# Kernel optimization log

Hardware: AMD Instinct MI355X
Metric: run time of the kernel (lower is better)

## Reference

```python
import jax, jax.numpy as jnp
import numpy as np

D_MODEL = 1024
N_HEADS = 16
D_HEAD = D_MODEL // N_HEADS
B, T = 4, 2048


def setup_inputs() -> dict:
    key = jax.random.key(0)
    ks = jax.random.split(key, 7)
    s = 0.02
    q = jax.random.normal(ks[0], (B, T, D_MODEL), dtype=jnp.float32)
    k = jax.random.normal(ks[1], (B, T, D_MODEL), dtype=jnp.float32)
    v = jax.random.normal(ks[2], (B, T, D_MODEL), dtype=jnp.float32)
    # causal mask, True = masked (strict upper triangle)
    mask = jnp.triu(jnp.ones((T, T), dtype=bool), k=1)[None, None, :, :]
    Wq = jax.random.normal(ks[3], (D_MODEL, D_MODEL), dtype=jnp.float32) * s
    Wk = jax.random.normal(ks[4], (D_MODEL, D_MODEL), dtype=jnp.float32) * s
    Wv = jax.random.normal(ks[5], (D_MODEL, D_MODEL), dtype=jnp.float32) * s
    Wo = jax.random.normal(ks[6], (D_MODEL, D_MODEL), dtype=jnp.float32) * s
    return {"q": q, "k": k, "v": v, "mask": mask,
            "Wq": Wq, "Wk": Wk, "Wv": Wv, "Wo": Wo}


def reference(q, k, v, mask, Wq, Wk, Wv, Wo):
    H, Dh = N_HEADS, D_HEAD
    scale = Dh ** -0.5

    def split(t):  # [B,T,D] -> [B,H,T,Dh]
        Bt, Tt, _ = t.shape
        return t.reshape(Bt, Tt, H, Dh).transpose(0, 2, 1, 3)

    # torch Linear (no bias): y = x @ W.T
    Q = split(q @ Wq.T)
    K = split(k @ Wk.T)
    V = split(v @ Wv.T)

    scores = jnp.einsum('bhqd,bhkd->bhqk', Q, K) * scale
    scores = jnp.where(mask, -jnp.inf, scores)
    attn = jax.nn.softmax(scores, axis=-1)
    attn = jnp.nan_to_num(attn)  # fully-masked rows -> 0
    out = jnp.einsum('bhqk,bhkd->bhqd', attn, V)
    out = out.transpose(0, 2, 1, 3).reshape(q.shape[0], q.shape[1], H * Dh)
    return out @ Wo.T
```

## Files before the change

### kernel.cpp

```cpp
#include <hip/hip_runtime.h>
#include <stdint.h>

#define D_MODEL 1024
#define N_HEADS 16
#define D_HEAD 64
#define BATCH 4
#define SEQ 2048
#define MTOT (BATCH * SEQ)

typedef unsigned short u16;
typedef __attribute__((ext_vector_type(8))) short bf16x8;
typedef __attribute__((ext_vector_type(4))) float f32x4;

#define MFMA(a, b, c) __builtin_amdgcn_mfma_f32_16x16x32_bf16((a), (b), (c), 0, 0, 0)
#define LOG2E 1.4426950408889634f
#define SC (0.125f * LOG2E)

static __device__ __forceinline__ u16 f2bf(float f) {
  unsigned u = __builtin_bit_cast(unsigned, f);
  u += 0x7fffu + ((u >> 16) & 1u);
  return (u16)(u >> 16);
}
static __device__ __forceinline__ u16 f2bf_t(float f) {
  return (u16)(__builtin_bit_cast(unsigned, f) >> 16);
}

static __device__ __forceinline__ void gload_lds16(const void* g, void* l) {
  __builtin_amdgcn_global_load_lds(
      (const __attribute__((address_space(1))) void*)g,
      (__attribute__((address_space(3))) void*)l, 16, 0, 0);
}

__global__ __launch_bounds__(256) void cvt3(const float* __restrict__ a,
                                            const float* __restrict__ b,
                                            const float* __restrict__ c,
                                            u16* __restrict__ oa, u16* __restrict__ ob,
                                            u16* __restrict__ oc) {
  const int z = blockIdx.y;
  const float* in = (z == 0) ? a : (z == 1) ? b : c;
  u16* out = (z == 0) ? oa : (z == 1) ? ob : oc;
  int i = blockIdx.x * 256 + threadIdx.x;
  float4 v = ((const float4*)in)[i];
  ushort4 o;
  o.x = f2bf(v.x); o.y = f2bf(v.y); o.z = f2bf(v.z); o.w = f2bf(v.w);
  ((ushort4*)out)[i] = o;
}

__global__ __launch_bounds__(256) void cvt4(const float* __restrict__ a,
                                            const float* __restrict__ b,
                                            const float* __restrict__ c,
                                            const float* __restrict__ d,
                                            u16* __restrict__ oa, u16* __restrict__ ob,
                                            u16* __restrict__ oc, u16* __restrict__ od) {
  const int z = blockIdx.y;
  const float* in = (z == 0) ? a : (z == 1) ? b : (z == 2) ? c : d;
  u16* out = (z == 0) ? oa : (z == 1) ? ob : (z == 2) ? oc : od;
  const float s = (z == 0) ? SC : 1.0f;
  int i = blockIdx.x * 256 + threadIdx.x;
  float4 v = ((const float4*)in)[i];
  ushort4 o;
  o.x = f2bf(v.x * s); o.y = f2bf(v.y * s); o.z = f2bf(v.z * s); o.w = f2bf(v.w * s);
  ((ushort4*)out)[i] = o;
}

#define BM 256
#define BN 128
#define BK 64
#define NKT (D_MODEL / BK)
#define ASZ (BM * BK)
#define BSZ (BN * BK)

static __device__ __forceinline__ void gemm_core(const u16* __restrict__ A,
                                                 const u16* __restrict__ B,
                                                 u16* As, u16* Bs,
                                                 int m0, int n0, f32x4 acc[4][4]) {
  const int t = threadIdx.x;
  const int lane = t & 63, wave = t >> 6;
  const int wm = wave >> 1, wn = wave & 1;
  const int lrow = lane & 15, quad = lane >> 4;
  const int srow = t >> 3;
  const int swcol = (((t & 7) ^ (srow & 7)) << 3);
  const int sdst = srow * 64 + (t & 7) * 8;
  const int rsw = lrow & 7;

#pragma unroll
  for (int i = 0; i < 4; i++)
#pragma unroll
    for (int j = 0; j < 4; j++) acc[i][j] = (f32x4){0.f, 0.f, 0.f, 0.f};

#define STAGE_(kt_, bi_)                                                        \
  do {                                                                          \
    const int k0_ = (kt_)*BK;                                                   \
    u16* as_ = As + (bi_)*ASZ;                                                  \
    u16* bs_ = Bs + (bi_)*BSZ;                                                  \
    _Pragma("unroll") for (int r_ = 0; r_ < 4; ++r_)                            \
        gload_lds16(A + (size_t)(m0 + r_ * 64 + srow) * 1024 + k0_ + swcol,     \
                    as_ + r_ * 64 * 64 + sdst);                                 \
    _Pragma("unroll") for (int r_ = 0; r_ < 2; ++r_)                            \
        gload_lds16(B + (size_t)(n0 + r_ * 64 + srow) * 1024 + k0_ + swcol,     \
                    bs_ + r_ * 64 * 64 + sdst);                                 \
  } while (0)

  STAGE_(0, 0);
  STAGE_(1, 1);

  for (int kt = 0; kt < NKT; ++kt) {
    if (kt < NKT - 1) asm volatile("s_waitcnt vmcnt(6)" ::: "memory");
    else              asm volatile("s_waitcnt vmcnt(0)" ::: "memory");
    __builtin_amdgcn_s_barrier();
    asm volatile("" ::: "memory");

    if (kt + 2 < NKT) STAGE_(kt + 2, (kt + 2) % 3);

    const u16* as = As + (kt % 3) * ASZ;
    const u16* bs = Bs + (kt % 3) * BSZ;

    bf16x8 a[2][4], b[2][4];
#pragma unroll
    for (int ks = 0; ks < 2; ++ks) {
      const int cx = ((ks * 4 + quad) ^ rsw) << 3;
#pragma unroll
      for (int i = 0; i < 4; i++)
        a[ks][i] = *(const bf16x8*)(as + (wm * 64 + i * 16 + lrow) * 64 + cx);
#pragma unroll
      for (int j = 0; j < 4; j++)
        b[ks][j] = *(const bf16x8*)(bs + (wn * 64 + j * 16 + lrow) * 64 + cx);
    }
    __builtin_amdgcn_sched_barrier(0);

    __builtin_amdgcn_s_setprio(1);
#pragma unroll
    for (int ks = 0; ks < 2; ++ks)
#pragma unroll
      for (int i = 0; i < 4; i++)
#pragma unroll
        for (int j = 0; j < 4; j++) acc[i][j] = MFMA(a[ks][i], b[ks][j], acc[i][j]);
    __builtin_amdgcn_s_setprio(0);
    __builtin_amdgcn_sched_barrier(0);
  }
#undef STAGE_
}

__global__ __launch_bounds__(512, 2) void gemm_qkv(const u16* __restrict__ xq,
                                                   const u16* __restrict__ xk,
                                                   const u16* __restrict__ xv,
                                                   const u16* __restrict__ Wqb,
                                                   const u16* __restrict__ Wkb,
                                                   const u16* __restrict__ Wvb,
                                                   u16* __restrict__ Qb, u16* __restrict__ Kb,
                                                   u16* __restrict__ Vtg, int zbase) {
  __shared__ u16 As[3 * ASZ];
  __shared__ u16 Bs[3 * BSZ];
  const int z = blockIdx.z + zbase;
  const u16* A = (z == 0) ? xq : (z == 1) ? xk : xv;
  const u16* B = (z == 0) ? Wqb : (z == 1) ? Wkb : Wvb;
  const int m0 = blockIdx.x * BM, n0 = blockIdx.y * BN;

  f32x4 acc[4][4];
  gemm_core(A, B, As, Bs, m0, n0, acc);

  const int lane = threadIdx.x & 63, wave = threadIdx.x >> 6;
  const int wm = wave >> 1, wn = wave & 1;
  const int lrow = lane & 15, quad = lane >> 4;

  if (z == 2) {
    const int b = m0 >> 11;
    const int t0 = (m0 & 2047);
#pragma unroll
    for (int i = 0; i < 4; i++) {
      const int trow = t0 + wm * 64 + i * 16 + quad * 4;
#pragma unroll
      for (int j = 0; j < 4; j++) {
        const int n = n0 + wn * 64 + j * 16 + lrow;
        ushort4 pk;
        pk.x = f2bf(acc[i][j][0]); pk.y = f2bf(acc[i][j][1]);
        pk.z = f2bf(acc[i][j][2]); pk.w = f2bf(acc[i][j][3]);
        *(ushort4*)(Vtg + (size_t)b * D_MODEL * SEQ + (size_t)n * SEQ + trow) = pk;
      }
    }
  } else {
    u16* C = z ? Kb : Qb;
#pragma unroll
    for (int i = 0; i < 4; i++) {
      const int mr = m0 + wm * 64 + i * 16 + quad * 4;
#pragma unroll
      for (int j = 0; j < 4; j++) {
        const int n = n0 + wn * 64 + j * 16 + lrow;
#pragma unroll
        for (int r = 0; r < 4; r++) C[(size_t)(mr + r) * 1024 + n] = f2bf(acc[i][j][r]);
      }
    }
  }
}

__global__ __launch_bounds__(512, 2) void gemm_o(const u16* __restrict__ A,
                                                 const u16* __restrict__ B,
                                                 float* __restrict__ C) {
  __shared__ u16 As[3 * ASZ];
  __shared__ u16 Bs[3 * BSZ];
  const int m0 = blockIdx.x * BM, n0 = blockIdx.y * BN;

  f32x4 acc[4][4];
  gemm_core(A, B, As, Bs, m0, n0, acc);

  const int lane = threadIdx.x & 63, wave = threadIdx.x >> 6;
  const int wm = wave >> 1, wn = wave & 1;
  const int lrow = lane & 15, quad = lane >> 4;
#pragma unroll
  for (int i = 0; i < 4; i++) {
    const int mr = m0 + wm * 64 + i * 16 + quad * 4;
#pragma unroll
    for (int j = 0; j < 4; j++) {
      const int n = n0 + wn * 64 + j * 16 + lrow;
#pragma unroll
      for (int r = 0; r < 4; r++) C[(size_t)(mr + r) * 1024 + n] = acc[i][j][r];
    }
  }
}

__global__ __launch_bounds__(256) void attn_causal(const u16* __restrict__ Qb,
                                                   const u16* __restrict__ Kb,
                                                   const u16* __restrict__ Vtg,
                                                   u16* __restrict__ Ob) {
  __shared__ u16 QPs[128 * 64];
  __shared__ u16 Ks[3 * 64 * 64];
  __shared__ u16 Vs[3 * 64 * 64];

  const int t = threadIdx.x;
  const int lane = t & 63, wave = t >> 6;
  const int lrow = lane & 15, quad = lane >> 4;
  const int wb = wave * 32;
  const int bh = blockIdx.x;
  const int b = bh >> 4, h = bh & 15;
  const int col0 = h * 64;
  const size_t rowbase = (size_t)b * SEQ;
  const size_t vbase = (size_t)b * (size_t)D_MODEL * SEQ;
  const int srow = t >> 3;
  const int swcol = (((t & 7) ^ (srow & 7)) << 3);
  const int pchunk = (t & 7) * 8;
  const int rsw = lrow & 7;

#define KVSTAGE_(kt_, bi_)                                                      \
  do {                                                                          \
    const int j0_ = (kt_)*64;                                                   \
    u16* ks_ = Ks + (bi_)*4096;                                                 \
    u16* vs_ = Vs + (bi_)*4096;                                                 \
    _Pragma("unroll") for (int r_ = 0; r_ < 2; ++r_) {                          \
      int rr_ = r_ * 32 + srow;                                                 \
      gload_lds16(Kb + (rowbase + j0_ + rr_) * D_MODEL + col0 + swcol,          \
                  ks_ + rr_ * 64 + pchunk);                                     \
      gload_lds16(Vtg + vbase + (size_t)(col0 + rr_) * SEQ + j0_ + swcol,       \
                  vs_ + rr_ * 64 + pchunk);                                     \
    }                                                                           \
  } while (0)

  bf16x8 bOnes;
  {
    const short ov = (lrow == 0) ? (short)0x3F80 : (short)0;
#pragma unroll
    for (int e = 0; e < 8; ++e) bOnes[e] = ov;
  }

  for (int part = 0; part < 2; ++part) {
    const int qt = part ? (15 - (int)blockIdx.y) : (int)blockIdx.y;
    const int qrow0 = qt * 128;
    const int nkt = 2 * qt + 2;

#pragma unroll
    for (int r = 0; r < 4; ++r) {
      int rr = r * 32 + srow;
      gload_lds16(Qb + (rowbase + qrow0 + rr) * D_MODEL + col0 + swcol,
                  QPs + rr * 64 + pchunk);
    }
    KVSTAGE_(0, 0);
    KVSTAGE_(1, 1);

    bf16x8 bQ[2][2];
    f32x4 oacc[2][4];
    f32x4 lacc[2];
#pragma unroll
    for (int mf = 0; mf < 2; mf++) {
#pragma unroll
      for (int df = 0; df < 4; df++) oacc[mf][df] = (f32x4){0.f, 0.f, 0.f, 0.f};
      lacc[mf] = (f32x4){0.f, 0.f, 0.f, 0.f};
    }

    for (int kt = 0; kt < nkt; ++kt) {
      if (kt < nkt - 1) asm volatile("s_waitcnt vmcnt(4)" ::: "memory");
      else              asm volatile("s_waitcnt vmcnt(0)" ::: "memory");
      __builtin_amdgcn_s_barrier();
      asm volatile("" ::: "memory");

      if (kt + 2 < nkt) KVSTAGE_(kt + 2, (kt + 2) % 3);

      const u16* ksb = Ks + (kt % 3) * 4096;
      const u16* vsb = Vs + (kt % 3) * 4096;

      if (kt == 0) {
#pragma unroll
        for (int mf = 0; mf < 2; ++mf)
#pragma unroll
          for (int ks = 0; ks < 2; ++ks)
            bQ[mf][ks] = *(const bf16x8*)(QPs + (wb + mf * 16 + lrow) * 64 +
                                          (((ks * 4 + quad) ^ rsw) << 3));
      }

      const int j0 = kt * 64;
      const bool diag = (kt >= 2 * qt);
#pragma unroll
      for (int mf = 0; mf < 2; ++mf) {
        f32x4 st[4];
#pragma unroll
        for (int jf = 0; jf < 4; jf++) st[jf] = (f32x4){0.f, 0.f, 0.f, 0.f};
#pragma unroll
        for (int ks = 0; ks < 2; ++ks) {
          const int cx = ((ks * 4 + quad) ^ rsw) << 3;
#pragma unroll
          for (int jf = 0; jf < 4; jf++) {
            bf16x8 aK = *(const bf16x8*)(ksb + (jf * 16 + lrow) * 64 + cx);
            st[jf] = MFMA(aK, bQ[mf][ks], st[jf]);
          }
        }
        const int m = wb + mf * 16 + lrow;
        const int gm = qrow0 + m;
#pragma unroll
        for (int jf = 0; jf < 4; jf++) {
          ushort4 pk;
#pragma unroll
          for (int r = 0; r < 4; r++) {
            float p = __builtin_amdgcn_exp2f(st[jf][r]);
            const int gj = j0 + jf * 16 + quad * 4 + r;
            if (diag && gj > gm) p = 0.f;
            ((u16*)&pk)[r] = f2bf_t(p);
          }
          const int j = jf * 16 + quad * 4;
          *(ushort4*)(QPs + m * 64 + ((((j >> 3) ^ (m & 7)) << 3) | (j & 7))) = pk;
        }
      }

#pragma unroll
      for (int ks = 0; ks < 2; ++ks) {
        const int cx = ((ks * 4 + quad) ^ rsw) << 3;
        bf16x8 aP[2];
#pragma unroll
        for (int mf = 0; mf < 2; ++mf)
          aP[mf] = *(const bf16x8*)(QPs + (wb + mf * 16 + lrow) * 64 + cx);
        lacc[0] = MFMA(aP[0], bOnes, lacc[0]);
        lacc[1] = MFMA(aP[1], bOnes, lacc[1]);
#pragma unroll
        for (int df = 0; df < 4; df++) {
          bf16x8 bV = *(const bf16x8*)(vsb + (df * 16 + lrow) * 64 + cx);
          oacc[0][df] = MFMA(aP[0], bV, oacc[0][df]);
          oacc[1][df] = MFMA(aP[1], bV, oacc[1][df]);
        }
      }
      __builtin_amdgcn_sched_barrier(0);
    }
    __syncthreads();

    float linv[2][4];
#pragma unroll
    for (int mf = 0; mf < 2; mf++)
#pragma unroll
      for (int r = 0; r < 4; r++)
        linv[mf][r] = 1.0f / __shfl(lacc[mf][r], lane & 48);

#pragma unroll
    for (int mf = 0; mf < 2; mf++)
#pragma unroll
      for (int r = 0; r < 4; r++) {
        u16* orow = Ob + (rowbase + qrow0 + wb + mf * 16 + quad * 4 + r) * D_MODEL + col0;
#pragma unroll
        for (int df = 0; df < 4; df++)
          orow[df * 16 + lrow] = f2bf(oacc[mf][df][r] * linv[mf][r]);
      }
  }
#undef KVSTAGE_
}

extern "C" void kernel_launch(void* const* d_in, const int* in_sizes, int n_in,
                              void* d_out, int out_size, void* d_ws, size_t ws_size,
                              hipStream_t stream) {
  const float* q  = (const float*)d_in[0];
  const float* k  = (const float*)d_in[1];
  const float* v  = (const float*)d_in[2];
  const float* Wq = (const float*)d_in[4];
  const float* Wk = (const float*)d_in[5];
  const float* Wv = (const float*)d_in[6];
  const float* Wo = (const float*)d_in[7];
  float* out = (float*)d_out;

  char* ws = (char*)d_ws;
  const size_t MB = 1 << 20;
  u16* xq  = (u16*)(ws);
  u16* xk  = (u16*)(ws + 16 * MB);
  u16* xv  = (u16*)(ws + 32 * MB);
  u16* Wqb = (u16*)(ws + 48 * MB);
  u16* Wkb = (u16*)(ws + 50 * MB);
  u16* Wvb = (u16*)(ws + 52 * MB);
  u16* Wob = (u16*)(ws + 54 * MB);
  u16* Qb  = (u16*)(ws + 56 * MB);

  const dim3 cb(256);
  const dim3 gb(512);
  cvt3<<<dim3(MTOT * D_MODEL / 4 / 256, 3), cb, 0, stream>>>(q, k, v, xq, xk, xv);
  cvt4<<<dim3(D_MODEL * D_MODEL / 4 / 256, 4), cb, 0, stream>>>(Wq, Wk, Wv, Wo,
                                                                Wqb, Wkb, Wvb, Wob);

  if (ws_size >= 104 * MB) {
    u16* Kb  = (u16*)(ws + 72 * MB);
    u16* Vtg = (u16*)(ws + 88 * MB);
    gemm_qkv<<<dim3(32, 8, 3), gb, 0, stream>>>(xq, xk, xv, Wqb, Wkb, Wvb,
                                                Qb, Kb, Vtg, 0);
    attn_causal<<<dim3(64, 8), cb, 0, stream>>>(Qb, Kb, Vtg, xq);
    gemm_o<<<dim3(32, 8), gb, 0, stream>>>(xq, Wob, out);
  } else {
    u16* Kb  = (u16*)(ws);
    u16* Vtg = (u16*)(ws + 16 * MB);
    u16* Oatt = (u16*)(ws + 32 * MB);
    gemm_qkv<<<dim3(32, 8, 1), gb, 0, stream>>>(xq, xq, xq, Wqb, Wqb, Wqb,
                                                Qb, Qb, Qb, 0);
    gemm_qkv<<<dim3(32, 8, 1), gb, 0, stream>>>(xk, xk, xk, Wkb, Wkb, Wkb,
                                                Kb, Kb, Kb, 1);
    gemm_qkv<<<dim3(32, 8, 1), gb, 0, stream>>>(xv, xv, xv, Wvb, Wvb, Wvb,
                                                Vtg, Vtg, Vtg, 2);
    attn_causal<<<dim3(64, 8), cb, 0, stream>>>(Qb, Kb, Vtg, Oatt);
    gemm_o<<<dim3(32, 8), gb, 0, stream>>>(Oatt, Wob, out);
  }
}
```

Before: 317.5 us.

## Enlarge GEMM tiles to 256x256 with double-buffered interleaved prefetch

Widens the projection GEMM block tile from 256x128 to 256x256, with 8 waves arranged 2x4 and each wave computing a 128x64 sub-tile, which raises arithmetic intensity per LDS load. The triple-buffered two-ahead prefetch becomes double buffering, with the next k-tile's global-to-LDS loads split into four chunks interleaved between MFMA phases. Grid blocks are halved (32x4), so there are fewer workgroups to fill the CUs. Accumulator registers double, which risks occupancy or spills, and the full vmcnt(0) wait each iteration may expose load latency.

```diff
diff --git a/kernel.cpp b/kernel.cpp
--- a/kernel.cpp
+++ b/kernel.cpp
@@ -64,19 +64,18 @@
 }
 
 #define BM 256
-#define BN 128
+#define BN 256
 #define BK 64
 #define NKT (D_MODEL / BK)
-#define ASZ (BM * BK)
-#define BSZ (BN * BK)
+#define TSZ (256 * 64)
 
 static __device__ __forceinline__ void gemm_core(const u16* __restrict__ A,
                                                  const u16* __restrict__ B,
                                                  u16* As, u16* Bs,
-                                                 int m0, int n0, f32x4 acc[4][4]) {
+                                                 int m0, int n0, f32x4 acc[8][4]) {
   const int t = threadIdx.x;
   const int lane = t & 63, wave = t >> 6;
-  const int wm = wave >> 1, wn = wave & 1;
+  const int wm = wave >> 2, wn = wave & 3;
   const int lrow = lane & 15, quad = lane >> 4;
   const int srow = t >> 3;
   const int swcol = (((t & 7) ^ (srow & 7)) << 3);
@@ -84,61 +83,94 @@
   const int rsw = lrow & 7;
 
 #pragma unroll
-  for (int i = 0; i < 4; i++)
+  for (int i = 0; i < 8; i++)
 #pragma unroll
     for (int j = 0; j < 4; j++) acc[i][j] = (f32x4){0.f, 0.f, 0.f, 0.f};
 
-#define STAGE_(kt_, bi_)                                                        \
-  do {                                                                          \
-    const int k0_ = (kt_)*BK;                                                   \
-    u16* as_ = As + (bi_)*ASZ;                                                  \
-    u16* bs_ = Bs + (bi_)*BSZ;                                                  \
-    _Pragma("unroll") for (int r_ = 0; r_ < 4; ++r_)                            \
-        gload_lds16(A + (size_t)(m0 + r_ * 64 + srow) * 1024 + k0_ + swcol,     \
-                    as_ + r_ * 64 * 64 + sdst);                                 \
-    _Pragma("unroll") for (int r_ = 0; r_ < 2; ++r_)                            \
-        gload_lds16(B + (size_t)(n0 + r_ * 64 + srow) * 1024 + k0_ + swcol,     \
-                    bs_ + r_ * 64 * 64 + sdst);                                 \
-  } while (0)
-
-  STAGE_(0, 0);
-  STAGE_(1, 1);
+#define SA_(kt_, bi_, r_)                                                       \
+  gload_lds16(A + (size_t)(m0 + (r_)*64 + srow) * 1024 + (kt_)*BK + swcol,      \
+              As + (bi_)*TSZ + (r_)*4096 + sdst)
+#define SB_(kt_, bi_, r_)                                                       \
+  gload_lds16(B + (size_t)(n0 + (r_)*64 + srow) * 1024 + (kt_)*BK + swcol,      \
+              Bs + (bi_)*TSZ + (r_)*4096 + sdst)
+
+#pragma unroll
+  for (int r = 0; r < 4; ++r) { SA_(0, 0, r); SB_(0, 0, r); }
 
   for (int kt = 0; kt < NKT; ++kt) {
-    if (kt < NKT - 1) asm volatile("s_waitcnt vmcnt(6)" ::: "memory");
-    else              asm volatile("s_waitcnt vmcnt(0)" ::: "memory");
+    asm volatile("s_waitcnt vmcnt(0)" ::: "memory");
     __builtin_amdgcn_s_barrier();
     asm volatile("" ::: "memory");
 
-    if (kt + 2 < NKT) STAGE_(kt + 2, (kt + 2) % 3);
-
-    const u16* as = As + (kt % 3) * ASZ;
-    const u16* bs = Bs + (kt % 3) * BSZ;
-
-    bf16x8 a[2][4], b[2][4];
-#pragma unroll
-    for (int ks = 0; ks < 2; ++ks) {
-      const int cx = ((ks * 4 + quad) ^ rsw) << 3;
-#pragma unroll
-      for (int i = 0; i < 4; i++)
-        a[ks][i] = *(const bf16x8*)(as + (wm * 64 + i * 16 + lrow) * 64 + cx);
-#pragma unroll
-      for (int j = 0; j < 4; j++)
-        b[ks][j] = *(const bf16x8*)(bs + (wn * 64 + j * 16 + lrow) * 64 + cx);
-    }
-    __builtin_amdgcn_sched_barrier(0);
-
+    const u16* as = As + (kt & 1) * TSZ;
+    const u16* bs = Bs + (kt & 1) * TSZ;
+    const int nb = (kt + 1) & 1;
+    const bool pf = (kt + 1 < NKT);
+    const int cx0 = (quad ^ rsw) << 3;
+    const int cx1 = ((4 + quad) ^ rsw) << 3;
+
+    bf16x8 a[4], b0[4], b1[4];
+
+    if (pf) { SA_(kt + 1, nb, 0); SB_(kt + 1, nb, 0); }
+#pragma unroll
+    for (int i = 0; i < 4; i++)
+      a[i] = *(const bf16x8*)(as + (wm * 128 + i * 16 + lrow) * 64 + cx0);
+#pragma unroll
+    for (int j = 0; j < 4; j++)
+      b0[j] = *(const bf16x8*)(bs + (wn * 64 + j * 16 + lrow) * 64 + cx0);
+    __builtin_amdgcn_sched_barrier(0);
     __builtin_amdgcn_s_setprio(1);
 #pragma unroll
-    for (int ks = 0; ks < 2; ++ks)
-#pragma unroll
-      for (int i = 0; i < 4; i++)
-#pragma unroll
-        for (int j = 0; j < 4; j++) acc[i][j] = MFMA(a[ks][i], b[ks][j], acc[i][j]);
+    for (int i = 0; i < 4; i++)
+#pragma unroll
+      for (int j = 0; j < 4; j++) acc[i][j] = MFMA(a[i], b0[j], acc[i][j]);
     __builtin_amdgcn_s_setprio(0);
     __builtin_amdgcn_sched_barrier(0);
-  }
-#undef STAGE_
+
+    if (pf) { SA_(kt + 1, nb, 1); SB_(kt + 1, nb, 1); }
+#pragma unroll
+    for (int i = 0; i < 4; i++)
+      a[i] = *(const bf16x8*)(as + (wm * 128 + (i + 4) * 16 + lrow) * 64 + cx0);
+    __builtin_amdgcn_sched_barrier(0);
+    __builtin_amdgcn_s_setprio(1);
+#pragma unroll
+    for (int i = 0; i < 4; i++)
+#pragma unroll
+      for (int j = 0; j < 4; j++) acc[i + 4][j] = MFMA(a[i], b0[j], acc[i + 4][j]);
+    __builtin_amdgcn_s_setprio(0);
+    __builtin_amdgcn_sched_barrier(0);
+
+    if (pf) { SA_(kt + 1, nb, 2); SB_(kt + 1, nb, 2); }
+#pragma unroll
+    for (int i = 0; i < 4; i++)
+      a[i] = *(const bf16x8*)(as + (wm * 128 + i * 16 + lrow) * 64 + cx1);
+#pragma unroll
+    for (int j = 0; j < 4; j++)
+      b1[j] = *(const bf16x8*)(bs + (wn * 64 + j * 16 + lrow) * 64 + cx1);
+    __builtin_amdgcn_sched_barrier(0);
+    __builtin_amdgcn_s_setprio(1);
+#pragma unroll
+    for (int i = 0; i < 4; i++)
+#pragma unroll
+      for (int j = 0; j < 4; j++) acc[i][j] = MFMA(a[i], b1[j], acc[i][j]);
+    __builtin_amdgcn_s_setprio(0);
+    __builtin_amdgcn_sched_barrier(0);
+
+    if (pf) { SA_(kt + 1, nb, 3); SB_(kt + 1, nb, 3); }
+#pragma unroll
+    for (int i = 0; i < 4; i++)
+      a[i] = *(const bf16x8*)(as + (wm * 128 + (i + 4) * 16 + lrow) * 64 + cx1);
+    __builtin_amdgcn_sched_barrier(0);
+    __builtin_amdgcn_s_setprio(1);
+#pragma unroll
+    for (int i = 0; i < 4; i++)
+#pragma unroll
+      for (int j = 0; j < 4; j++) acc[i + 4][j] = MFMA(a[i], b1[j], acc[i + 4][j]);
+    __builtin_amdgcn_s_setprio(0);
+    __builtin_amdgcn_sched_barrier(0);
+  }
+#undef SA_
+#undef SB_
 }
 
 __global__ __launch_bounds__(512, 2) void gemm_qkv(const u16* __restrict__ xq,
@@ -149,26 +181,26 @@
                                                    const u16* __restrict__ Wvb,
                                                    u16* __restrict__ Qb, u16* __restrict__ Kb,
                                                    u16* __restrict__ Vtg, int zbase) {
-  __shared__ u16 As[3 * ASZ];
-  __shared__ u16 Bs[3 * BSZ];
+  __shared__ u16 As[2 * TSZ];
+  __shared__ u16 Bs[2 * TSZ];
   const int z = blockIdx.z + zbase;
   const u16* A = (z == 0) ? xq : (z == 1) ? xk : xv;
   const u16* B = (z == 0) ? Wqb : (z == 1) ? Wkb : Wvb;
   const int m0 = blockIdx.x * BM, n0 = blockIdx.y * BN;
 
-  f32x4 acc[4][4];
+  f32x4 acc[8][4];
   gemm_core(A, B, As, Bs, m0, n0, acc);
 
   const int lane = threadIdx.x & 63, wave = threadIdx.x >> 6;
-  const int wm = wave >> 1, wn = wave & 1;
+  const int wm = wave >> 2, wn = wave & 3;
   const int lrow = lane & 15, quad = lane >> 4;
 
   if (z == 2) {
     const int b = m0 >> 11;
     const int t0 = (m0 & 2047);
 #pragma unroll
-    for (int i = 0; i < 4; i++) {
-      const int trow = t0 + wm * 64 + i * 16 + quad * 4;
+    for (int i = 0; i < 8; i++) {
+      const int trow = t0 + wm * 128 + i * 16 + quad * 4;
 #pragma unroll
       for (int j = 0; j < 4; j++) {
         const int n = n0 + wn * 64 + j * 16 + lrow;
@@ -181,8 +213,8 @@
   } else {
     u16* C = z ? Kb : Qb;
 #pragma unroll
-    for (int i = 0; i < 4; i++) {
-      const int mr = m0 + wm * 64 + i * 16 + quad * 4;
+    for (int i = 0; i < 8; i++) {
+      const int mr = m0 + wm * 128 + i * 16 + quad * 4;
 #pragma unroll
       for (int j = 0; j < 4; j++) {
         const int n = n0 + wn * 64 + j * 16 + lrow;
@@ -196,19 +228,19 @@
 __global__ __launch_bounds__(512, 2) void gemm_o(const u16* __restrict__ A,
                                                  const u16* __restrict__ B,
                                                  float* __restrict__ C) {
-  __shared__ u16 As[3 * ASZ];
-  __shared__ u16 Bs[3 * BSZ];
+  __shared__ u16 As[2 * TSZ];
+  __shared__ u16 Bs[2 * TSZ];
   const int m0 = blockIdx.x * BM, n0 = blockIdx.y * BN;
 
-  f32x4 acc[4][4];
+  f32x4 acc[8][4];
   gemm_core(A, B, As, Bs, m0, n0, acc);
 
   const int lane = threadIdx.x & 63, wave = threadIdx.x >> 6;
-  const int wm = wave >> 1, wn = wave & 1;
+  const int wm = wave >> 2, wn = wave & 3;
   const int lrow = lane & 15, quad = lane >> 4;
 #pragma unroll
-  for (int i = 0; i < 4; i++) {
-    const int mr = m0 + wm * 64 + i * 16 + quad * 4;
+  for (int i = 0; i < 8; i++) {
+    const int mr = m0 + wm * 128 + i * 16 + quad * 4;
 #pragma unroll
     for (int j = 0; j < 4; j++) {
       const int n = n0 + wn * 64 + j * 16 + lrow;
@@ -410,21 +442,21 @@
   if (ws_size >= 104 * MB) {
     u16* Kb  = (u16*)(ws + 72 * MB);
     u16* Vtg = (u16*)(ws + 88 * MB);
-    gemm_qkv<<<dim3(32, 8, 3), gb, 0, stream>>>(xq, xk, xv, Wqb, Wkb, Wvb,
+    gemm_qkv<<<dim3(32, 4, 3), gb, 0, stream>>>(xq, xk, xv, Wqb, Wkb, Wvb,
                                                 Qb, Kb, Vtg, 0);
     attn_causal<<<dim3(64, 8), cb, 0, stream>>>(Qb, Kb, Vtg, xq);
-    gemm_o<<<dim3(32, 8), gb, 0, stream>>>(xq, Wob, out);
+    gemm_o<<<dim3(32, 4), gb, 0, stream>>>(xq, Wob, out);
   } else {
     u16* Kb  = (u16*)(ws);
     u16* Vtg = (u16*)(ws + 16 * MB);
     u16* Oatt = (u16*)(ws + 32 * MB);
-    gemm_qkv<<<dim3(32, 8, 1), gb, 0, stream>>>(xq, xq, xq, Wqb, Wqb, Wqb,
+    gemm_qkv<<<dim3(32, 4, 1), gb, 0, stream>>>(xq, xq, xq, Wqb, Wqb, Wqb,
                                                 Qb, Qb, Qb, 0);
-    gemm_qkv<<<dim3(32, 8, 1), gb, 0, stream>>>(xk, xk, xk, Wkb, Wkb, Wkb,
+    gemm_qkv<<<dim3(32, 4, 1), gb, 0, stream>>>(xk, xk, xk, Wkb, Wkb, Wkb,
                                                 Kb, Kb, Kb, 1);
-    gemm_qkv<<<dim3(32, 8, 1), gb, 0, stream>>>(xv, xv, xv, Wvb, Wvb, Wvb,
+    gemm_qkv<<<dim3(32, 4, 1), gb, 0, stream>>>(xv, xv, xv, Wvb, Wvb, Wvb,
                                                 Vtg, Vtg, Vtg, 2);
     attn_causal<<<dim3(64, 8), cb, 0, stream>>>(Qb, Kb, Vtg, Oatt);
-    gemm_o<<<dim3(32, 8), gb, 0, stream>>>(Oatt, Wob, out);
-  }
-}
+    gemm_o<<<dim3(32, 4), gb, 0, stream>>>(Oatt, Wob, out);
+  }
+}
```

After: 348.1 us. 9.6% more time.
